# Performance work log

Measured on AMD Instinct MI355X. Metric: run time of the kernel, lower is better.

The kernel has to match this reference:

```python
import jax, jax.numpy as jnp
import numpy as np
import math

N_HEADS = 8
LN_EPS = 1e-5


def _segment_softmax(att, seg, n):
    # att: [E, H], seg: [E] target-node ids; grouped softmax over edges per target node
    m = jax.ops.segment_max(att, seg, num_segments=n)
    e = jnp.exp(att - m[seg])
    d = jax.ops.segment_sum(e, seg, num_segments=n)
    return e / (d[seg] + 1e-16)


def _layernorm(h, g, b):
    mu = jnp.mean(h, axis=-1, keepdims=True)
    var = jnp.mean((h - mu) ** 2, axis=-1, keepdims=True)
    return (h - mu) * jax.lax.rsqrt(var + LN_EPS) * g + b


def setup_inputs() -> dict:
    key = jax.random.key(0)
    ks = jax.random.split(key, 16)
    T, N, E, Din, Dh = 3, 20000, 100000, 128, 128
    s = 0.02
    x = jax.random.normal(ks[0], (T, N, Din), dtype=jnp.float32)
    edge_index = jax.random.randint(ks[1], (T, 2, E), 0, N, dtype=jnp.int64)
    return {
        "x": x,
        "edge_index": edge_index,
        "Wq": jax.random.normal(ks[2], (Din, Dh), jnp.float32) * s,
        "bq": jnp.zeros((Dh,), jnp.float32),
        "Wk": jax.random.normal(ks[3], (Din, Dh), jnp.float32) * s,
        "bk": jnp.zeros((Dh,), jnp.float32),
        "Wv": jax.random.normal(ks[4], (Din, Dh), jnp.float32) * s,
        "bv": jnp.zeros((Dh,), jnp.float32),
        "ln_g": jnp.ones((Dh,), jnp.float32),
        "ln_b": jnp.zeros((Dh,), jnp.float32),
        "W1": jax.random.normal(ks[5], (Dh, 2 * Dh), jnp.float32) * s,
        "b1": jnp.zeros((2 * Dh,), jnp.float32),
        "W2": jax.random.normal(ks[6], (2 * Dh, Dh), jnp.float32) * s,
        "b2": jnp.zeros((Dh,), jnp.float32),
    }


def reference(x, edge_index, Wq, bq, Wk, bk, Wv, bv, ln_g, ln_b, W1, b1, W2, b2):
    T, N, _ = x.shape
    Dh = Wq.shape[1]
    dk = Dh // N_HEADS
    inv_sqrt_dk = 1.0 / math.sqrt(dk)

    def ffn(h):
        r = _layernorm(h, ln_g, ln_b)
        r = jax.nn.gelu(r @ W1 + b1, approximate=False)
        r = r @ W2 + b2
        return h + r

    xs, cs, ss = [], [], []
    for t_tar in range(T):
        x_tar = x[t_tar]  # [N, Din]
        # collect edges of times 0..t_tar
        tgt = jnp.concatenate([edge_index[t, 1] for t in range(t_tar + 1)])  # [Ec]
        x_tar_e = x_tar[tgt]  # [Ec, Din]
        x_src_e = jnp.concatenate(
            [x[t][edge_index[t, 0]] for t in range(t_tar + 1)], axis=0
        )  # [Ec, Din]

        q = (x_tar_e @ Wq + bq).reshape(-1, N_HEADS, dk)
        k = (x_src_e @ Wk + bk).reshape(-1, N_HEADS, dk)
        v = (x_src_e @ Wv + bv).reshape(-1, N_HEADS, dk)
        att = jnp.sum(q * k, axis=-1) * inv_sqrt_dk  # [Ec, H]

        res_att = _segment_softmax(att, tgt, N)
        spu_att = _segment_softmax(-att, tgt, N)
        res = (v * res_att[..., None]).reshape(-1, Dh)
        spu = (v * spu_att[..., None]).reshape(-1, Dh)
        causal_hat = jax.ops.segment_sum(res, tgt, num_segments=N)
        spurious_hat = jax.ops.segment_sum(spu, tgt, num_segments=N)

        causal = ffn(causal_hat + x_tar)
        spurious = ffn(spurious_hat)
        xs.append(causal + spurious)
        cs.append(causal)
        ss.append(spurious)
    return (jnp.stack(xs), jnp.stack(cs), jnp.stack(ss))
```

## Files before the change

kernel.cpp:

```cpp
#include <hip/hip_runtime.h>
#include <hip/hip_bf16.h>

#define DEV_INLINE __device__ __forceinline__

namespace {

constexpr int T = 3;
constexpr int NN = 20000;
constexpr int NE = 100000;
constexpr int D = 128;
constexpr int D2 = 256;
constexpr int NROW = T * NN;
constexpr size_t OUTSZ = (size_t)T * NN * D;

typedef __attribute__((ext_vector_type(8))) short bf16x8;
typedef __attribute__((ext_vector_type(4))) float f32x4;
typedef __attribute__((ext_vector_type(2))) _Float16 h2;
typedef __hip_bfloat16 bf16;

DEV_INLINE unsigned short f2bf(float f) {
  __hip_bfloat16 t = __float2bfloat16(f);
  return *(unsigned short*)&t;
}

__global__ void k_detect(const unsigned int* __restrict__ ei32, int* __restrict__ flag) {
  int nz = 0;
  for (int i = threadIdx.x; i < 4096; i += 256)
    nz |= (ei32[2 * i + 1] != 0u);
  if (__any(nz) && (threadIdx.x & 63) == 0) atomicOr(&flag[0], 1);
}

DEV_INLINE int loadIdx(const void* ei, int is32, long long idx) {
  return is32 ? ((const int*)ei)[idx] : (int)((const long long*)ei)[idx];
}

__global__ void k_count(const void* __restrict__ ei, const int* __restrict__ flag,
                        int* __restrict__ counts) {
  int i = blockIdx.x * blockDim.x + threadIdx.x;
  if (i >= T * NE) return;
  int is32 = flag[0];
  int t = i / NE, e = i - t * NE;
  int tgt = loadIdx(ei, is32, (long long)(t * 2 + 1) * NE + e);
  atomicAdd(&counts[t * NN + tgt], 1);
}

__global__ void k_scan(const int* __restrict__ counts, int* __restrict__ offsets,
                       int* __restrict__ cursor) {
  int t = blockIdx.x;
  const int* c = counts + t * NN;
  int* o = offsets + t * (NN + 1);
  int* cur = cursor + t * NN;
  __shared__ int part[256];
  int tid = threadIdx.x;
  constexpr int CH = (NN + 255) / 256;
  int b = tid * CH;
  int e = min(b + CH, NN);
  int s = 0;
  for (int i = b; i < e; i++) s += c[i];
  part[tid] = s;
  __syncthreads();
  for (int d = 1; d < 256; d <<= 1) {
    int v = (tid >= d) ? part[tid - d] : 0;
    __syncthreads();
    part[tid] += v;
    __syncthreads();
  }
  int run = part[tid] - s;
  for (int i = b; i < e; i++) { o[i] = run; cur[i] = run; run += c[i]; }
  if (tid == 255) o[NN] = part[255];
}

__global__ void k_scatter(const void* __restrict__ ei, const int* __restrict__ flag,
                          int* __restrict__ cursor, int* __restrict__ elist) {
  int i = blockIdx.x * blockDim.x + threadIdx.x;
  if (i >= T * NE) return;
  int is32 = flag[0];
  int t = i / NE, e = i - t * NE;
  int src = loadIdx(ei, is32, (long long)(t * 2 + 0) * NE + e);
  int tgt = loadIdx(ei, is32, (long long)(t * 2 + 1) * NE + e);
  int pos = atomicAdd(&cursor[t * NN + tgt], 1);
  elist[t * NE + pos] = src;
}

__global__ void k_precast(const float* __restrict__ Wq, const float* __restrict__ Wk,
                          const float* __restrict__ Wv, const float* __restrict__ W1,
                          const float* __restrict__ W2, bf16* __restrict__ WqkvT,
                          bf16* __restrict__ W1T, bf16* __restrict__ W2T) {
  int i0 = blockIdx.x * blockDim.x + threadIdx.x;
  int stride = gridDim.x * blockDim.x;
  for (int j = i0; j < 384 * 128; j += stride) {
    int c = j >> 7, k = j & 127;
    float v = c < 128 ? Wq[k * D + c]
                      : (c < 256 ? Wk[k * D + (c - 128)] : Wv[k * D + (c - 256)]);
    WqkvT[c * 128 + k] = __float2bfloat16(v);
  }
  for (int j = i0; j < 256 * 128; j += stride) {
    int c = j >> 7, k = j & 127;
    W1T[c * 128 + k] = __float2bfloat16(W1[k * D2 + c]);
  }
  for (int j = i0; j < 128 * 256; j += stride) {
    int c = j >> 8, k = j & 255;
    W2T[c * 256 + k] = __float2bfloat16(W2[k * D + c]);
  }
}

__global__ __launch_bounds__(256) void k_qkv_mfma(
    const float* __restrict__ x, const bf16* __restrict__ WqkvT,
    const float* __restrict__ bq, const float* __restrict__ bk,
    const float* __restrict__ bv,
    _Float16* __restrict__ Qh, _Float16* __restrict__ Kh, _Float16* __restrict__ Vh) {
  __shared__ char As[64 * 256];
  __shared__ char Bs[384 * 80];
  int row0 = blockIdx.x * 64;
  int tid = threadIdx.x;
  for (int i = tid; i < 64 * 16; i += 256) {
    int rr = i >> 4, kb = i & 15;
    int grow = row0 + rr;
    uint4 v = make_uint4(0, 0, 0, 0);
    if (grow < NROW) {
      float4 lo = *(const float4*)&x[(size_t)grow * D + kb * 8];
      float4 hi = *(const float4*)&x[(size_t)grow * D + kb * 8 + 4];
      v.x = ((unsigned)f2bf(lo.y) << 16) | f2bf(lo.x);
      v.y = ((unsigned)f2bf(lo.w) << 16) | f2bf(lo.z);
      v.z = ((unsigned)f2bf(hi.y) << 16) | f2bf(hi.x);
      v.w = ((unsigned)f2bf(hi.w) << 16) | f2bf(hi.z);
    }
    *(uint4*)(As + rr * 256 + ((kb * 16) ^ ((rr & 7) << 4))) = v;
  }
  int wid = tid >> 6, lane = tid & 63;
  int lr = lane & 15, lg = lane >> 4;
  f32x4 acc[24];
#pragma unroll
  for (int i = 0; i < 24; i++) acc[i] = (f32x4){0.f, 0.f, 0.f, 0.f};
  for (int kk = 0; kk < 4; kk++) {
    __syncthreads();
    for (int i = tid; i < 384 * 4; i += 256) {
      int c = i >> 2, ko = (i & 3) * 8;
      *(uint4*)(Bs + c * 80 + ko * 2) =
          *(const uint4*)&WqkvT[(size_t)c * 128 + kk * 32 + ko];
    }
    __syncthreads();
    int ar = wid * 16 + lr;
    bf16x8 a = *(bf16x8*)(As + ar * 256 + ((kk * 64 + lg * 16) ^ ((ar & 7) << 4)));
#pragma unroll
    for (int nt = 0; nt < 24; nt++) {
      bf16x8 b = *(bf16x8*)(Bs + (nt * 16 + lr) * 80 + lg * 16);
      acc[nt] = __builtin_amdgcn_mfma_f32_16x16x32_bf16(a, b, acc[nt], 0, 0, 0);
    }
  }
#pragma unroll
  for (int nt = 0; nt < 24; nt++) {
    int m = nt >> 3;
    int c = (nt & 7) * 16 + lr;
    const float* bias = m == 0 ? bq : (m == 1 ? bk : bv);
    _Float16* dst = m == 0 ? Qh : (m == 1 ? Kh : Vh);
    float scale = m == 0 ? 0.25f : 1.f;
    float bb = bias[c];
#pragma unroll
    for (int j = 0; j < 4; j++) {
      int orow = row0 + wid * 16 + lg * 4 + j;
      if (orow < NROW) dst[(size_t)orow * D + c] = (_Float16)((acc[nt][j] + bb) * scale);
    }
  }
}

DEV_INLINE float waveReduceSum(float v) {
#pragma unroll
  for (int m = 1; m < 64; m <<= 1) v += __shfl_xor(v, m, 64);
  return v;
}

template <bool B0, bool B1, bool B2>
DEV_INLINE void edgeUpdate(h2 q0, h2 q1, h2 q2, unsigned kraw, unsigned vraw,
                           float& dr0, float& ds0, float& arx0, float& ary0,
                           float& asx0, float& asy0, float& dr1, float& ds1,
                           float& arx1, float& ary1, float& asx1, float& asy1,
                           float& dr2, float& ds2, float& arx2, float& ary2,
                           float& asx2, float& asy2) {
  h2 kh = __builtin_bit_cast(h2, kraw);
  h2 vh = __builtin_bit_cast(h2, vraw);
  float vx = (float)vh[0], vy = (float)vh[1];
  float a0 = 0.f, a1 = 0.f, a2 = 0.f;
  if (B0) a0 = __builtin_amdgcn_fdot2(q0, kh, 0.f, false);
  if (B1) a1 = __builtin_amdgcn_fdot2(q1, kh, 0.f, false);
  if (B2) a2 = __builtin_amdgcn_fdot2(q2, kh, 0.f, false);
  if (B0) a0 += __shfl_xor(a0, 1, 64);
  if (B1) a1 += __shfl_xor(a1, 1, 64);
  if (B2) a2 += __shfl_xor(a2, 1, 64);
  if (B0) a0 += __shfl_xor(a0, 2, 64);
  if (B1) a1 += __shfl_xor(a1, 2, 64);
  if (B2) a2 += __shfl_xor(a2, 2, 64);
  if (B0) a0 += __shfl_xor(a0, 4, 64);
  if (B1) a1 += __shfl_xor(a1, 4, 64);
  if (B2) a2 += __shfl_xor(a2, 4, 64);
  if (B0) {
    float e = __expf(a0), f = __expf(-a0);
    dr0 += e; arx0 += e * vx; ary0 += e * vy;
    ds0 += f; asx0 += f * vx; asy0 += f * vy;
  }
  if (B1) {
    float e = __expf(a1), f = __expf(-a1);
    dr1 += e; arx1 += e * vx; ary1 += e * vy;
    ds1 += f; asx1 += f * vx; asy1 += f * vy;
  }
  if (B2) {
    float e = __expf(a2), f = __expf(-a2);
    dr2 += e; arx2 += e * vx; ary2 += e * vy;
    ds2 += f; asx2 += f * vx; asy2 += f * vy;
  }
}

__global__ __launch_bounds__(256) void k_attn(
    const _Float16* __restrict__ Qh, const _Float16* __restrict__ Kh,
    const _Float16* __restrict__ Vh, const float* __restrict__ x,
    const int* __restrict__ offsets, const int* __restrict__ elist,
    const float* __restrict__ lng, const float* __restrict__ lnb,
    float* __restrict__ h, bf16* __restrict__ rb) {
  int n = blockIdx.x * 4 + (threadIdx.x >> 6);
  int l = threadIdx.x & 63;
  float2 g2 = *(const float2*)&lng[2 * l];
  float2 b2 = *(const float2*)&lnb[2 * l];
  h2 q0 = __builtin_bit_cast(h2, *(const unsigned*)&Qh[((size_t)0 * NN + n) * D + 2 * l]);
  h2 q1 = __builtin_bit_cast(h2, *(const unsigned*)&Qh[((size_t)1 * NN + n) * D + 2 * l]);
  h2 q2 = __builtin_bit_cast(h2, *(const unsigned*)&Qh[((size_t)2 * NN + n) * D + 2 * l]);
  float dr0 = 0.f, ds0 = 0.f, arx0 = 0.f, ary0 = 0.f, asx0 = 0.f, asy0 = 0.f;
  float dr1 = 0.f, ds1 = 0.f, arx1 = 0.f, ary1 = 0.f, asx1 = 0.f, asy1 = 0.f;
  float dr2 = 0.f, ds2 = 0.f, arx2 = 0.f, ary2 = 0.f, asx2 = 0.f, asy2 = 0.f;
#define TSEC(TT, B0, B1, B2)                                                    \
  {                                                                             \
    const int* off = offsets + TT * (NN + 1);                                   \
    int b = off[n], e = off[n + 1];                                             \
    const int* el = elist + TT * NE;                                            \
    const _Float16* Kt = Kh + (size_t)TT * NN * D;                              \
    const _Float16* Vt = Vh + (size_t)TT * NN * D;                              \
    for (int i = b; i < e; i++) {                                               \
      int s = el[i];                                                            \
      size_t ai = (size_t)s * D + 2 * l;                                        \
      unsigned kraw = *(const unsigned*)&Kt[ai];                                \
      unsigned vraw = *(const unsigned*)&Vt[ai];                                \
      edgeUpdate<B0, B1, B2>(q0, q1, q2, kraw, vraw, dr0, ds0, arx0, ary0,      \
                             asx0, asy0, dr1, ds1, arx1, ary1, asx1, asy1,      \
                             dr2, ds2, arx2, ary2, asx2, asy2);                 \
    }                                                                           \
  }
  TSEC(0, true, true, true)
  TSEC(1, false, true, true)
  TSEC(2, false, false, true)
#undef TSEC
#define EPILOGUE(TT, DR, DS, ARX, ARY, ASX, ASY)                                 \
  {                                                                              \
    float2 xr = *(const float2*)&x[((size_t)TT * NN + n) * D + 2 * l];           \
    float ir = 1.f / (DR + 1e-16f), is = 1.f / (DS + 1e-16f);                    \
    float hcx = ARX * ir + xr.x, hcy = ARY * ir + xr.y;                          \
    float hsx = ASX * is, hsy = ASY * is;                                        \
    float mu = waveReduceSum(hcx + hcy) * (1.f / 128.f);                         \
    float dx = hcx - mu, dy = hcy - mu;                                          \
    float var = waveReduceSum(dx * dx + dy * dy) * (1.f / 128.f);                \
    float rstd = rsqrtf(var + 1e-5f);                                            \
    float rcx = dx * rstd * g2.x + b2.x, rcy = dy * rstd * g2.y + b2.y;          \
    float mu2 = waveReduceSum(hsx + hsy) * (1.f / 128.f);                        \
    float ex = hsx - mu2, ey = hsy - mu2;                                        \
    float var2 = waveReduceSum(ex * ex + ey * ey) * (1.f / 128.f);               \
    float rstd2 = rsqrtf(var2 + 1e-5f);                                          \
    float rsx = ex * rstd2 * g2.x + b2.x, rsy = ey * rstd2 * g2.y + b2.y;        \
    size_t base = (size_t)TT * 2 * NN;                                           \
    size_t iC = (base + n) * D + 2 * l;                                          \
    size_t iS = (base + NN + n) * D + 2 * l;                                     \
    *(float2*)&h[iC] = make_float2(hcx, hcy);                                    \
    *(float2*)&h[iS] = make_float2(hsx, hsy);                                    \
    *(unsigned*)&rb[iC] = ((unsigned)f2bf(rcy) << 16) | f2bf(rcx);               \
    *(unsigned*)&rb[iS] = ((unsigned)f2bf(rsy) << 16) | f2bf(rsx);               \
  }
  EPILOGUE(0, dr0, ds0, arx0, ary0, asx0, asy0)
  EPILOGUE(1, dr1, ds1, arx1, ary1, asx1, asy1)
  EPILOGUE(2, dr2, ds2, arx2, ary2, asx2, asy2)
#undef EPILOGUE
}

__global__ __launch_bounds__(256) void k_ffn_fused(
    const bf16* __restrict__ rb, const bf16* __restrict__ W1T,
    const float* __restrict__ b1, const bf16* __restrict__ W2T,
    const float* __restrict__ b2, const float* __restrict__ h,
    float* __restrict__ out) {
  __shared__ char As[32 * 256];
  __shared__ char Gs[32 * 528];
  __shared__ char Bs[256 * 80];
  int blk = blockIdx.x;
  int t2 = blk / 1250;
  int n0 = (blk - t2 * 1250) * 16;
  size_t base = (size_t)t2 * 2 * NN;
  int tid = threadIdx.x;
  for (int i = tid; i < 32 * 16; i += 256) {
    int rr = i >> 4, kb = i & 15;
    size_t grow = base + (size_t)(rr >> 4) * NN + n0 + (rr & 15);
    *(uint4*)(As + rr * 256 + ((kb * 16) ^ ((rr & 7) << 4))) =
        *(const uint4*)&rb[grow * D + kb * 8];
  }
  int wid = tid >> 6, lane = tid & 63;
  int lr = lane & 15, lg = lane >> 4;
  int wr = (wid & 1) * 16;
  int wc1 = (wid >> 1) * 128;
  int wc2 = (wid >> 1) * 64;
  int ar = wr + lr;
  f32x4 acc1[8];
#pragma unroll
  for (int i = 0; i < 8; i++) acc1[i] = (f32x4){0.f, 0.f, 0.f, 0.f};
  for (int kk = 0; kk < 4; kk++) {
    __syncthreads();
    for (int i = tid; i < 256 * 4; i += 256) {
      int c = i >> 2, ko = (i & 3) * 8;
      *(uint4*)(Bs + c * 80 + ko * 2) =
          *(const uint4*)&W1T[(size_t)c * 128 + kk * 32 + ko];
    }
    __syncthreads();
    bf16x8 a = *(bf16x8*)(As + ar * 256 + ((kk * 64 + lg * 16) ^ ((ar & 7) << 4)));
#pragma unroll
    for (int nt = 0; nt < 8; nt++) {
      bf16x8 b = *(bf16x8*)(Bs + (wc1 + nt * 16 + lr) * 80 + lg * 16);
      acc1[nt] = __builtin_amdgcn_mfma_f32_16x16x32_bf16(a, b, acc1[nt], 0, 0, 0);
    }
  }
#pragma unroll
  for (int nt = 0; nt < 8; nt++) {
    int c = wc1 + nt * 16 + lr;
    float bb = b1[c];
#pragma unroll
    for (int j = 0; j < 4; j++) {
      int r = wr + lg * 4 + j;
      float y = acc1[nt][j] + bb;
      y = 0.5f * y * (1.f + erff(y * 0.70710678118654752f));
      unsigned us = f2bf(y);
      unsigned nb = __shfl_xor(us, 1, 64);
      if ((lr & 1) == 0) {
        *(unsigned*)(Gs + r * 528 + c * 2) = (nb << 16) | us;
      }
    }
  }
  f32x4 acc2[4];
#pragma unroll
  for (int i = 0; i < 4; i++) acc2[i] = (f32x4){0.f, 0.f, 0.f, 0.f};
  for (int kk = 0; kk < 8; kk++) {
    __syncthreads();
    for (int i = tid; i < 128 * 4; i += 256) {
      int c = i >> 2, ko = (i & 3) * 8;
      *(uint4*)(Bs + c * 80 + ko * 2) =
          *(const uint4*)&W2T[(size_t)c * 256 + kk * 32 + ko];
    }
    __syncthreads();
    bf16x8 a = *(bf16x8*)(Gs + ar * 528 + kk * 64 + lg * 16);
#pragma unroll
    for (int nt = 0; nt < 4; nt++) {
      bf16x8 b = *(bf16x8*)(Bs + (wc2 + nt * 16 + lr) * 80 + lg * 16);
      acc2[nt] = __builtin_amdgcn_mfma_f32_16x16x32_bf16(a, b, acc2[nt], 0, 0, 0);
    }
  }
  __syncthreads();
  float* zbuf = (float*)Gs;
#pragma unroll
  for (int nt = 0; nt < 4; nt++) {
    int c = wc2 + nt * 16 + lr;
    float bb = b2[c];
#pragma unroll
    for (int j = 0; j < 4; j++) {
      int rr = wr + lg * 4 + j;
      int side = rr >> 4;
      int node = n0 + (rr & 15);
      float z = acc2[nt][j] + bb + h[(base + (size_t)side * NN + node) * D + c];
      out[(size_t)(1 + side) * OUTSZ + ((size_t)t2 * NN + node) * D + c] = z;
      zbuf[rr * 128 + c] = z;
    }
  }
  __syncthreads();
  for (int i = tid; i < 16 * 128; i += 256) {
    int node = i >> 7, c = i & 127;
    out[((size_t)t2 * NN + n0 + node) * D + c] =
        zbuf[node * 128 + c] + zbuf[(node + 16) * 128 + c];
  }
}

}

extern "C" void kernel_launch(void* const* d_in, const int* in_sizes, int n_in,
                              void* d_out, int out_size, void* d_ws, size_t ws_size,
                              hipStream_t stream) {
  const float* x = (const float*)d_in[0];
  const void* ei = d_in[1];
  const float* Wq = (const float*)d_in[2];
  const float* bq = (const float*)d_in[3];
  const float* Wk = (const float*)d_in[4];
  const float* bk = (const float*)d_in[5];
  const float* Wv = (const float*)d_in[6];
  const float* bv = (const float*)d_in[7];
  const float* lng = (const float*)d_in[8];
  const float* lnb = (const float*)d_in[9];
  const float* W1 = (const float*)d_in[10];
  const float* b1 = (const float*)d_in[11];
  const float* W2 = (const float*)d_in[12];
  const float* b2 = (const float*)d_in[13];
  float* out = (float*)d_out;

  char* ws = (char*)d_ws;
  size_t off = 0;
  auto alloc = [&](size_t bytes) -> void* {
    void* p = ws + off;
    off += (bytes + 255) & ~(size_t)255;
    return p;
  };
  bf16* WqkvT = (bf16*)alloc((size_t)384 * 128 * 2);
  bf16* W1T = (bf16*)alloc((size_t)256 * 128 * 2);
  bf16* W2T = (bf16*)alloc((size_t)128 * 256 * 2);
  _Float16* Qh = (_Float16*)alloc((size_t)NROW * D * 2);
  _Float16* Kh = (_Float16*)alloc((size_t)NROW * D * 2);
  _Float16* Vh = (_Float16*)alloc((size_t)NROW * D * 2);
  float* h = (float*)alloc((size_t)T * 2 * NN * D * 4);
  bf16* rb = (bf16*)alloc((size_t)T * 2 * NN * D * 2);
  int* counts = (int*)alloc((size_t)T * NN * 4);
  int* offsets = (int*)alloc((size_t)T * (NN + 1) * 4);
  int* cursor = (int*)alloc((size_t)T * NN * 4);
  int* elist = (int*)alloc((size_t)T * NE * 4);
  int* dflag = (int*)alloc(256);

  hipMemsetAsync(counts, 0, (size_t)T * NN * 4, stream);
  hipMemsetAsync(dflag, 0, 8, stream);
  k_detect<<<1, 256, 0, stream>>>((const unsigned int*)ei, dflag);
  int eb = (T * NE + 255) / 256;
  k_count<<<eb, 256, 0, stream>>>(ei, dflag, counts);
  k_scan<<<T, 256, 0, stream>>>(counts, offsets, cursor);
  k_scatter<<<eb, 256, 0, stream>>>(ei, dflag, cursor, elist);
  k_precast<<<128, 256, 0, stream>>>(Wq, Wk, Wv, W1, W2, WqkvT, W1T, W2T);
  k_qkv_mfma<<<(NROW + 63) / 64, 256, 0, stream>>>(x, WqkvT, bq, bk, bv, Qh, Kh, Vh);
  k_attn<<<NN / 4, 256, 0, stream>>>(Qh, Kh, Vh, x, offsets, elist, lng, lnb, h, rb);
  k_ffn_fused<<<T * (NN / 16), 256, 0, stream>>>(rb, W1T, b1, W2T, b2, h, out);
}
```

Measured before the change: 299.9 us.

## Make FFN kernel persistent with weights resident in LDS and prefetched tiles

The FFN kernel becomes a persistent kernel: 256 blocks of 512 threads each load the full bf16 W1 and W2 (128 KB) into shared memory once. Each block then loops over node tiles, prefetching the next tile's activations into registers while computing the current one. This replaces the per-tile restaging of weight slices and the barriers that came with it. Weights are pre-laid out in k-chunk blocks so they can be copied straight into LDS, and the zbuf row stride is padded. The cost is about 150 KB of LDS per block, so one block per CU, and lower latency hiding from having fewer resident waves.

New measurement: 271.6 us. 1.1x faster.

```diff
diff --git a/kernel.cpp b/kernel.cpp
--- a/kernel.cpp
+++ b/kernel.cpp
@@ -12,6 +12,7 @@
 constexpr int D2 = 256;
 constexpr int NROW = T * NN;
 constexpr size_t OUTSZ = (size_t)T * NN * D;
+constexpr int NTILE = T * (NN / 16);
 
 typedef __attribute__((ext_vector_type(8))) short bf16x8;
 typedef __attribute__((ext_vector_type(4))) float f32x4;
@@ -85,7 +86,7 @@
 __global__ void k_precast(const float* __restrict__ Wq, const float* __restrict__ Wk,
                           const float* __restrict__ Wv, const float* __restrict__ W1,
                           const float* __restrict__ W2, bf16* __restrict__ WqkvT,
-                          bf16* __restrict__ W1T, bf16* __restrict__ W2T) {
+                          bf16* __restrict__ W1L, bf16* __restrict__ W2L) {
   int i0 = blockIdx.x * blockDim.x + threadIdx.x;
   int stride = gridDim.x * blockDim.x;
   for (int j = i0; j < 384 * 128; j += stride) {
@@ -94,13 +95,13 @@
                       : (c < 256 ? Wk[k * D + (c - 128)] : Wv[k * D + (c - 256)]);
     WqkvT[c * 128 + k] = __float2bfloat16(v);
   }
-  for (int j = i0; j < 256 * 128; j += stride) {
-    int c = j >> 7, k = j & 127;
-    W1T[c * 128 + k] = __float2bfloat16(W1[k * D2 + c]);
-  }
-  for (int j = i0; j < 128 * 256; j += stride) {
-    int c = j >> 8, k = j & 255;
-    W2T[c * 256 + k] = __float2bfloat16(W2[k * D + c]);
+  for (int idx = i0; idx < 4 * 256 * 32; idx += stride) {
+    int j = idx & 31, c = (idx >> 5) & 255, kk = idx >> 13;
+    W1L[idx] = __float2bfloat16(W1[(kk * 32 + j) * D2 + c]);
+  }
+  for (int idx = i0; idx < 8 * 128 * 32; idx += stride) {
+    int j = idx & 31, c = (idx >> 5) & 127, kk = idx >> 12;
+    W2L[idx] = __float2bfloat16(W2[(kk * 32 + j) * D + c]);
   }
 }
 
@@ -277,104 +278,110 @@
 #undef EPILOGUE
 }
 
-__global__ __launch_bounds__(256) void k_ffn_fused(
-    const bf16* __restrict__ rb, const bf16* __restrict__ W1T,
-    const float* __restrict__ b1, const bf16* __restrict__ W2T,
+__global__ __launch_bounds__(512) void k_ffn_fused(
+    const bf16* __restrict__ rb, const bf16* __restrict__ W1L,
+    const bf16* __restrict__ W2L, const float* __restrict__ b1,
     const float* __restrict__ b2, const float* __restrict__ h,
     float* __restrict__ out) {
+  __shared__ char W1s[65536];
+  __shared__ char W2s[65536];
   __shared__ char As[32 * 256];
   __shared__ char Gs[32 * 528];
-  __shared__ char Bs[256 * 80];
-  int blk = blockIdx.x;
-  int t2 = blk / 1250;
-  int n0 = (blk - t2 * 1250) * 16;
-  size_t base = (size_t)t2 * 2 * NN;
   int tid = threadIdx.x;
-  for (int i = tid; i < 32 * 16; i += 256) {
-    int rr = i >> 4, kb = i & 15;
-    size_t grow = base + (size_t)(rr >> 4) * NN + n0 + (rr & 15);
-    *(uint4*)(As + rr * 256 + ((kb * 16) ^ ((rr & 7) << 4))) =
-        *(const uint4*)&rb[grow * D + kb * 8];
-  }
+  for (int i = tid; i < 4096; i += 512)
+    *(uint4*)(W1s + i * 16) = *(const uint4*)((const char*)W1L + i * 16);
+  for (int i = tid; i < 4096; i += 512)
+    *(uint4*)(W2s + i * 16) = *(const uint4*)((const char*)W2L + i * 16);
   int wid = tid >> 6, lane = tid & 63;
   int lr = lane & 15, lg = lane >> 4;
   int wr = (wid & 1) * 16;
-  int wc1 = (wid >> 1) * 128;
-  int wc2 = (wid >> 1) * 64;
+  int wc1 = (wid >> 1) * 64;
+  int wc2 = (wid >> 1) * 32;
   int ar = wr + lr;
-  f32x4 acc1[8];
-#pragma unroll
-  for (int i = 0; i < 8; i++) acc1[i] = (f32x4){0.f, 0.f, 0.f, 0.f};
-  for (int kk = 0; kk < 4; kk++) {
-    __syncthreads();
-    for (int i = tid; i < 256 * 4; i += 256) {
-      int c = i >> 2, ko = (i & 3) * 8;
-      *(uint4*)(Bs + c * 80 + ko * 2) =
-          *(const uint4*)&W1T[(size_t)c * 128 + kk * 32 + ko];
-    }
-    __syncthreads();
-    bf16x8 a = *(bf16x8*)(As + ar * 256 + ((kk * 64 + lg * 16) ^ ((ar & 7) << 4)));
-#pragma unroll
-    for (int nt = 0; nt < 8; nt++) {
-      bf16x8 b = *(bf16x8*)(Bs + (wc1 + nt * 16 + lr) * 80 + lg * 16);
-      acc1[nt] = __builtin_amdgcn_mfma_f32_16x16x32_bf16(a, b, acc1[nt], 0, 0, 0);
-    }
-  }
-#pragma unroll
-  for (int nt = 0; nt < 8; nt++) {
-    int c = wc1 + nt * 16 + lr;
-    float bb = b1[c];
-#pragma unroll
-    for (int j = 0; j < 4; j++) {
-      int r = wr + lg * 4 + j;
-      float y = acc1[nt][j] + bb;
-      y = 0.5f * y * (1.f + erff(y * 0.70710678118654752f));
-      unsigned us = f2bf(y);
-      unsigned nb = __shfl_xor(us, 1, 64);
-      if ((lr & 1) == 0) {
-        *(unsigned*)(Gs + r * 528 + c * 2) = (nb << 16) | us;
+  int srr = tid >> 4, skb = tid & 15;
+  float bb1[4], bb2[2];
+#pragma unroll
+  for (int nt = 0; nt < 4; nt++) bb1[nt] = b1[wc1 + nt * 16 + lr];
+#pragma unroll
+  for (int nt = 0; nt < 2; nt++) bb2[nt] = b2[wc2 + nt * 16 + lr];
+  int tile = blockIdx.x;
+  uint4 pref;
+  {
+    int t2 = tile / 1250, nb = tile - t2 * 1250;
+    size_t grow = (size_t)t2 * 2 * NN + (size_t)(srr >> 4) * NN + nb * 16 + (srr & 15);
+    pref = *(const uint4*)&rb[grow * D + skb * 8];
+  }
+  for (; tile < NTILE; tile += gridDim.x) {
+    int t2 = tile / 1250, nb = tile - t2 * 1250;
+    int n0 = nb * 16;
+    size_t base = (size_t)t2 * 2 * NN;
+    *(uint4*)(As + srr * 256 + ((skb * 16) ^ ((srr & 7) << 4))) = pref;
+    int ntile = tile + gridDim.x;
+    if (ntile < NTILE) {
+      int t2n = ntile / 1250, nbn = ntile - t2n * 1250;
+      size_t grow = (size_t)t2n * 2 * NN + (size_t)(srr >> 4) * NN + nbn * 16 + (srr & 15);
+      pref = *(const uint4*)&rb[grow * D + skb * 8];
+    }
+    __syncthreads();
+    f32x4 acc1[4];
+#pragma unroll
+    for (int i = 0; i < 4; i++) acc1[i] = (f32x4){0.f, 0.f, 0.f, 0.f};
+#pragma unroll
+    for (int kk = 0; kk < 4; kk++) {
+      bf16x8 a = *(bf16x8*)(As + ar * 256 + ((kk * 64 + lg * 16) ^ ((ar & 7) << 4)));
+#pragma unroll
+      for (int nt = 0; nt < 4; nt++) {
+        bf16x8 b = *(bf16x8*)(W1s + (kk * 256 + wc1 + nt * 16 + lr) * 64 + lg * 16);
+        acc1[nt] = __builtin_amdgcn_mfma_f32_16x16x32_bf16(a, b, acc1[nt], 0, 0, 0);
       }
     }
-  }
-  f32x4 acc2[4];
-#pragma unroll
-  for (int i = 0; i < 4; i++) acc2[i] = (f32x4){0.f, 0.f, 0.f, 0.f};
-  for (int kk = 0; kk < 8; kk++) {
-    __syncthreads();
-    for (int i = tid; i < 128 * 4; i += 256) {
-      int c = i >> 2, ko = (i & 3) * 8;
-      *(uint4*)(Bs + c * 80 + ko * 2) =
-          *(const uint4*)&W2T[(size_t)c * 256 + kk * 32 + ko];
-    }
-    __syncthreads();
-    bf16x8 a = *(bf16x8*)(Gs + ar * 528 + kk * 64 + lg * 16);
 #pragma unroll
     for (int nt = 0; nt < 4; nt++) {
-      bf16x8 b = *(bf16x8*)(Bs + (wc2 + nt * 16 + lr) * 80 + lg * 16);
-      acc2[nt] = __builtin_amdgcn_mfma_f32_16x16x32_bf16(a, b, acc2[nt], 0, 0, 0);
-    }
-  }
-  __syncthreads();
-  float* zbuf = (float*)Gs;
-#pragma unroll
-  for (int nt = 0; nt < 4; nt++) {
-    int c = wc2 + nt * 16 + lr;
-    float bb = b2[c];
-#pragma unroll
-    for (int j = 0; j < 4; j++) {
-      int rr = wr + lg * 4 + j;
-      int side = rr >> 4;
-      int node = n0 + (rr & 15);
-      float z = acc2[nt][j] + bb + h[(base + (size_t)side * NN + node) * D + c];
-      out[(size_t)(1 + side) * OUTSZ + ((size_t)t2 * NN + node) * D + c] = z;
-      zbuf[rr * 128 + c] = z;
-    }
-  }
-  __syncthreads();
-  for (int i = tid; i < 16 * 128; i += 256) {
-    int node = i >> 7, c = i & 127;
-    out[((size_t)t2 * NN + n0 + node) * D + c] =
-        zbuf[node * 128 + c] + zbuf[(node + 16) * 128 + c];
+      int c = wc1 + nt * 16 + lr;
+#pragma unroll
+      for (int j = 0; j < 4; j++) {
+        int r = wr + lg * 4 + j;
+        float y = acc1[nt][j] + bb1[nt];
+        y = 0.5f * y * (1.f + erff(y * 0.70710678118654752f));
+        unsigned us = f2bf(y);
+        unsigned nbv = __shfl_xor(us, 1, 64);
+        if ((lr & 1) == 0) *(unsigned*)(Gs + r * 528 + c * 2) = (nbv << 16) | us;
+      }
+    }
+    __syncthreads();
+    f32x4 acc2[2];
+#pragma unroll
+    for (int i = 0; i < 2; i++) acc2[i] = (f32x4){0.f, 0.f, 0.f, 0.f};
+#pragma unroll
+    for (int kk = 0; kk < 8; kk++) {
+      bf16x8 a = *(bf16x8*)(Gs + ar * 528 + kk * 64 + lg * 16);
+#pragma unroll
+      for (int nt = 0; nt < 2; nt++) {
+        bf16x8 b = *(bf16x8*)(W2s + (kk * 128 + wc2 + nt * 16 + lr) * 64 + lg * 16);
+        acc2[nt] = __builtin_amdgcn_mfma_f32_16x16x32_bf16(a, b, acc2[nt], 0, 0, 0);
+      }
+    }
+    __syncthreads();
+    float* zbuf = (float*)Gs;
+#pragma unroll
+    for (int nt = 0; nt < 2; nt++) {
+      int c = wc2 + nt * 16 + lr;
+#pragma unroll
+      for (int j = 0; j < 4; j++) {
+        int rr2 = wr + lg * 4 + j;
+        int side = rr2 >> 4;
+        int node = n0 + (rr2 & 15);
+        float z = acc2[nt][j] + bb2[nt] + h[(base + (size_t)side * NN + node) * D + c];
+        out[(size_t)(1 + side) * OUTSZ + ((size_t)t2 * NN + node) * D + c] = z;
+        zbuf[rr2 * 132 + c] = z;
+      }
+    }
+    __syncthreads();
+    for (int i = tid; i < 16 * 128; i += 512) {
+      int node = i >> 7, c = i & 127;
+      out[((size_t)t2 * NN + n0 + node) * D + c] =
+          zbuf[node * 132 + c] + zbuf[(node + 16) * 132 + c];
+    }
   }
 }
 
@@ -407,8 +414,8 @@
     return p;
   };
   bf16* WqkvT = (bf16*)alloc((size_t)384 * 128 * 2);
-  bf16* W1T = (bf16*)alloc((size_t)256 * 128 * 2);
-  bf16* W2T = (bf16*)alloc((size_t)128 * 256 * 2);
+  bf16* W1L = (bf16*)alloc((size_t)128 * 256 * 2);
+  bf16* W2L = (bf16*)alloc((size_t)256 * 128 * 2);
   _Float16* Qh = (_Float16*)alloc((size_t)NROW * D * 2);
   _Float16* Kh = (_Float16*)alloc((size_t)NROW * D * 2);
   _Float16* Vh = (_Float16*)alloc((size_t)NROW * D * 2);
@@ -427,8 +434,8 @@
   k_count<<<eb, 256, 0, stream>>>(ei, dflag, counts);
   k_scan<<<T, 256, 0, stream>>>(counts, offsets, cursor);
   k_scatter<<<eb, 256, 0, stream>>>(ei, dflag, cursor, elist);
-  k_precast<<<128, 256, 0, stream>>>(Wq, Wk, Wv, W1, W2, WqkvT, W1T, W2T);
+  k_precast<<<128, 256, 0, stream>>>(Wq, Wk, Wv, W1, W2, WqkvT, W1L, W2L);
   k_qkv_mfma<<<(NROW + 63) / 64, 256, 0, stream>>>(x, WqkvT, bq, bk, bv, Qh, Kh, Vh);
   k_attn<<<NN / 4, 256, 0, stream>>>(Qh, Kh, Vh, x, offsets, elist, lng, lnb, h, rb);
-  k_ffn_fused<<<T * (NN / 16), 256, 0, stream>>>(rb, W1T, b1, W2T, b2, h, out);
-}
+  k_ffn_fused<<<256, 512, 0, stream>>>(rb, W1L, W2L, b1, b2, h, out);
+}
```
